# Kernel optimization log

Measured on AMD Instinct MI355X. Metric: run time of the kernel, lower is better.

Reference implementation:

```python
import jax, jax.numpy as jnp
import numpy as np

# ---- dims ----
N = 16380      # atoms
R = 819        # residues
APR = 20       # atoms per residue
K = 16         # k_neighbors
H = 64         # hidden_mult (channels)
HEADS = 8
DH = H // HEADS
L = 6          # hidden_layers
BINS = 100
MIN_D, MAX_D = 0.0, 10.0
E_DIM = 64     # embed_dim
FFN = 2 * H    # mlp_ratio = 2


def setup_inputs() -> dict:
    key = jax.random.key(0)
    ks = jax.random.split(key, 22)
    g = lambda k, shape, fan: jax.random.normal(k, shape, jnp.float32) / np.sqrt(fan)
    return {
        'coords': jax.random.uniform(ks[0], (N, 3), jnp.float32) * 70.0,
        'atom_ids': jax.random.randint(ks[1], (N,), 0, 64),
        'res_ids': jax.random.randint(ks[2], (N,), 0, 8),
        'elem_ids': jax.random.randint(ks[3], (N,), 0, 16),
        'residue_index': jnp.repeat(jnp.arange(R), APR),
        'emb_atom': jax.random.normal(ks[4], (64, 32), jnp.float32),
        'emb_res': jax.random.normal(ks[5], (8, 16), jnp.float32),
        'emb_elem': jax.random.normal(ks[6], (16, 16), jnp.float32),
        'Win': g(ks[7], (E_DIM, H), E_DIM),
        'Wq': g(ks[8], (L, H, H), H),
        'Wk': g(ks[9], (L, H, H), H),
        'Wv': g(ks[10], (L, H, H), H),
        'Wvec': g(ks[11], (L, H, H), H),
        'wdir': jax.random.normal(ks[12], (L, H), jnp.float32) * 0.1,
        'dist_bias': jax.random.normal(ks[13], (L, BINS, HEADS), jnp.float32) * 0.1,
        'Wo': g(ks[14], (L, H, H), H),
        'W1': g(ks[15], (L, H, FFN), H),
        'W2': g(ks[16], (L, FFN, H), FFN),
        'Wg': g(ks[17], (L, H, H), H),
        'Wout': g(ks[18], (H, 2), H),
        'bout': jnp.zeros((2,), jnp.float32),
    }


def _ln(x):
    m = jnp.mean(x, axis=-1, keepdims=True)
    v = jnp.mean((x - m) ** 2, axis=-1, keepdims=True)
    return (x - m) * jax.lax.rsqrt(v + 1e-5)


def reference(coords, atom_ids, res_ids, elem_ids, residue_index,
              emb_atom, emb_res, emb_elem, Win, Wq, Wk, Wv, Wvec, wdir,
              dist_bias, Wo, W1, W2, Wg, Wout, bout):
    n = coords.shape[0]
    # --- polymer embedding: concat atom/residue/element embeddings ---
    feat = jnp.concatenate(
        [emb_atom[atom_ids], emb_res[res_ids], emb_elem[elem_ids]], axis=-1)  # (N, E_DIM)
    # --- kNN graph via dense pairwise distances (avoid (N,N,3) intermediate) ---
    sq = jnp.sum(coords * coords, axis=-1)
    d2 = sq[:, None] + sq[None, :] - 2.0 * (coords @ coords.T)     # (N, N)
    idx = jnp.arange(n)
    d2 = d2.at[idx, idx].set(jnp.inf)
    _, nbr = jax.lax.top_k(-d2, K)                                  # (N, K) src per dst
    # --- edge geometry: relative vector, distance, bin ---
    dvec = coords[:, None, :] - coords[nbr]                         # (N, K, 3) dst - src
    d = jnp.sqrt(jnp.sum(dvec * dvec, axis=-1) + 1e-12)
    dirn = dvec / d[..., None]
    bins = jnp.clip(((d - MIN_D) / (MAX_D - MIN_D) * BINS).astype(jnp.int32), 0, BINS - 1)
    # --- lift to hidden repr: scalars from embedding, vectors start at zero ---
    s = feat @ Win                                                  # (N, H) l=0 features
    v = jnp.zeros((n, H, 3), s.dtype)                               # (N, H, 3) l=1 features
    for l in range(L):
        h = _ln(s)
        q = (h @ Wq[l]).reshape(n, HEADS, DH)
        kf = (h @ Wk[l]).reshape(n, HEADS, DH)
        vf = (h @ Wv[l]).reshape(n, HEADS, DH)
        kn, vn = kf[nbr], vf[nbr]                                   # (N, K, HEADS, DH)
        logits = jnp.einsum('nhd,nkhd->nkh', q, kn) / np.sqrt(DH) + dist_bias[l][bins]
        attn = jax.nn.softmax(logits, axis=1)                       # softmax over K nbrs
        msg = jnp.einsum('nkh,nkhd->nhd', attn, vn).reshape(n, H)
        # equivariant vector messages: mixed source vectors + edge direction term
        vvals = jnp.einsum('nhc,hg->ngc', v, Wvec[l])               # (N, H, 3)
        vmsg = vvals[nbr] + wdir[l][None, None, :, None] * dirn[:, :, None, :]
        attn_c = jnp.repeat(attn, DH, axis=-1)                      # (N, K, H)
        vagg = jnp.einsum('nkh,nkhc->nhc', attn_c, vmsg)
        s = s + msg @ Wo[l]
        v = v + vagg
        h2 = _ln(s)
        s = s + jax.nn.gelu(h2 @ W1[l]) @ W2[l]                     # scalar FFN
        v = v * jax.nn.sigmoid(h2 @ Wg[l])[..., None]               # gated vector update
    # --- out repr is l=0 only; residue mean-pool then linear head ---
    res_feat = jax.ops.segment_sum(s, residue_index, num_segments=R) / APR
    return res_feat @ Wout + bout                                   # (R, 2)
```

## Files before the change

### kernel.cpp

```cpp
#include <hip/hip_runtime.h>
#include <cfloat>

#define NN    16380
#define RR    819
#define APR   20
#define KNB   16
#define HID   64
#define LAYERS 6
#define BINS  100
#define N64   (NN*HID)

#define ATB   32
#define NBLK  512
#define LDA   68
#define LDU   132
#define CSIZE 4.375f

#define OFF_QA    0
#define OFF_KA    (1*N64)
#define OFF_FA    (2*N64)
#define OFF_QB    (3*N64)
#define OFF_KB    (4*N64)
#define OFF_FB    (5*N64)
#define OFF_VA    (6*N64)
#define OFF_VB    (9*N64)
#define OFF_S     (12*N64)
#define OFF_DIRNS (13*N64)
#define OFF_C4    (OFF_DIRNS + NN*48)
#define OFF_C4S   (OFF_C4 + NN*4)
#define OFF_RES   (OFF_C4S + NN*4)
#define OFF_NBRS  (OFF_RES + RR*64)
#define OFF_BINSS (OFF_NBRS + NN*16)
#define OFF_O2N   (OFF_BINSS + NN*16)
#define OFF_N2O   (OFF_O2N + NN)
#define OFF_CELL  (OFF_N2O + NN)
#define OFF_HIST  (OFF_CELL + NN)
#define OFF_CNT   (OFF_HIST + 4096)
#define OFF_BASE  (OFF_CNT + 4096)

typedef unsigned long long u64;
#define U64MAX 0xFFFFFFFFFFFFFFFFull

__device__ __forceinline__ float gelu_f(float x) {
    float x3 = x*x*x;
    float t = tanhf(0.7978845608028654f*(x + 0.044715f*x3));
    return 0.5f*x*(1.0f+t);
}
__device__ __forceinline__ float sigmoid_f(float x) {
    return 1.0f/(1.0f + expf(-x));
}
__device__ __forceinline__ int spread3(int x) {
    return (x&1) | ((x&2)<<2) | ((x&4)<<4) | ((x&8)<<6);
}
__device__ __forceinline__ unsigned sortable_u32(float f) {
    unsigned u = __float_as_uint(f);
    return u ^ ((u & 0x80000000u) ? 0xFFFFFFFFu : 0x80000000u);
}

__global__ void pad_cell_kernel(const float* __restrict__ coords, float4* __restrict__ c4,
                                int* __restrict__ cellid, int* __restrict__ hist,
                                float* __restrict__ resb, int n) {
    int i = blockIdx.x*256 + threadIdx.x;
    for (int j = i; j < RR*HID; j += 16384) resb[j] = 0.f;
    if (i >= n) return;
    float x = coords[3*i], y = coords[3*i+1], z = coords[3*i+2];
    float sq = __fadd_rn(__fadd_rn(__fmul_rn(x,x), __fmul_rn(y,y)), __fmul_rn(z,z));
    c4[i] = make_float4(x, y, z, sq);
    int cx = min(15, max(0, (int)(x * (16.0f/70.0f))));
    int cy = min(15, max(0, (int)(y * (16.0f/70.0f))));
    int cz = min(15, max(0, (int)(z * (16.0f/70.0f))));
    int m = spread3(cx) | (spread3(cy)<<1) | (spread3(cz)<<2);
    cellid[i] = m;
    atomicAdd(&hist[m], 1);
}
__global__ void scan_kernel(const int* __restrict__ hist, int* __restrict__ base) {
    __shared__ int part[256];
    int t = threadIdx.x;
    int loc[16]; int s = 0;
    #pragma unroll
    for (int e = 0; e < 16; ++e) { loc[e] = s; s += hist[t*16+e]; }
    part[t] = s;
    __syncthreads();
    if (t == 0) { int acc = 0; for (int i = 0; i < 256; ++i) { int v = part[i]; part[i] = acc; acc += v; } }
    __syncthreads();
    int off = part[t];
    #pragma unroll
    for (int e = 0; e < 16; ++e) base[t*16+e] = off + loc[e];
}
__global__ void scatter_kernel(const int* __restrict__ cellid, const int* __restrict__ base,
                               int* __restrict__ cnt, int* __restrict__ o2n,
                               int* __restrict__ n2o, const float4* __restrict__ c4,
                               float4* __restrict__ c4s, int n) {
    int i = blockIdx.x*256 + threadIdx.x;
    if (i >= n) return;
    int m = cellid[i];
    int pos = base[m] + atomicAdd(&cnt[m], 1);
    o2n[i] = pos; n2o[pos] = i;
    c4s[pos] = c4[i];
}

#define SCRATCH 1024
__global__ __launch_bounds__(256) void knn_grid_kernel(
    const float4* __restrict__ c4s, const int* __restrict__ base, const int* __restrict__ hist,
    const int* __restrict__ n2o, const int* __restrict__ o2n,
    int* __restrict__ nbr, int* __restrict__ binsO, float* __restrict__ dirn, int n)
{
    __shared__ int sIdx[4][SCRATCH];
    int tid = threadIdx.x;
    int wv = tid >> 6, lane = tid & 63;
    int i = blockIdx.x*4 + wv;
    bool valid = i < n;
    int ii = valid ? i : 0;
    float4 cd = c4s[ii];
    float sqd = cd.w;
    int cx = min(15, max(0, (int)(cd.x * (16.0f/70.0f))));
    int cy = min(15, max(0, (int)(cd.y * (16.0f/70.0f))));
    int cz = min(15, max(0, (int)(cd.z * (16.0f/70.0f))));
    u64 dlist = U64MAX;
    u64 vmax  = U64MAX;
    int* sidx = sIdx[wv];

    auto compute_pk = [&](int idx) -> u64 {
        if (idx == i) return U64MAX;
        float4 cc = c4s[idx];
        float dt = __fmul_rn(cd.x, cc.x);
        dt = __fmaf_rn(cd.y, cc.y, dt);
        dt = __fmaf_rn(cd.z, cc.z, dt);
        float key = __fsub_rn(__fadd_rn(sqd, cc.w), __fmul_rn(2.0f, dt));
        int org = n2o[idx];
        return ((u64)sortable_u32(key) << 32) | (unsigned)org;
    };

    auto process_batch = [&](int M) {
        if (M <= 0) return;
        u64 lmin = U64MAX;
        for (int p = lane; p < M; p += 64) {
            u64 pk = compute_pk(sidx[p]);
            lmin = (pk < lmin) ? pk : lmin;
        }
        u64 T = lmin;
        #pragma unroll
        for (int off = 1; off < 64; off <<= 1) {
            u64 o = __shfl_xor(T, off);
            T = (o > T) ? o : T;
        }
        for (int c0 = 0; c0 < M; c0 += 64) {
            int p = c0 + lane;
            u64 mypk = (p < M) ? compute_pk(sidx[p]) : U64MAX;
            u64 bound = (vmax < T) ? vmax : T;
            unsigned long long mask = __ballot(mypk <= bound);
            while (mask) {
                int lb = (int)__builtin_ctzll(mask);
                mask &= mask - 1;
                u64 dc = __shfl(mypk, lb);
                if (dc < vmax) {
                    u64 dp = __shfl_up(dlist, 1);
                    bool below = dc < dlist;
                    bool take  = below && (lane == 0 || dc >= dp);
                    if (lane < 16) dlist = below ? (take ? dc : dp) : dlist;
                    vmax = __shfl(dlist, 15);
                }
            }
        }
    };

    for (int R = 2; R <= 16; ++R) {
        int side = 2*R+1;
        int ncell = side*side*side;
        int M = 0;
        for (int t0 = 0; t0 < ncell; t0 += 64) {
            int t = t0 + lane;
            int cnt = 0, b = 0;
            if (t < ncell) {
                int dxc = t % side - R;
                int dyc = (t/side) % side - R;
                int dzc = t/(side*side) - R;
                int ch = max(abs(dxc), max(abs(dyc), abs(dzc)));
                bool use = (R == 2) || (ch == R);
                int x = cx+dxc, y = cy+dyc, z = cz+dzc;
                if (use && x>=0 && x<16 && y>=0 && y<16 && z>=0 && z<16) {
                    int m = spread3(x) | (spread3(y)<<1) | (spread3(z)<<2);
                    cnt = hist[m]; b = base[m];
                }
            }
            int incl = cnt;
            #pragma unroll
            for (int o = 1; o < 64; o <<= 1) { int v = __shfl_up(incl, o); if (lane >= o) incl += v; }
            int excl = incl - cnt;
            int tot = __shfl(incl, 63);
            if (M + tot > SCRATCH) { process_batch(M); M = 0; }
            for (int e = 0; e < cnt; ++e) {
                int pos = M + excl + e;
                if (pos < SCRATCH) sidx[pos] = b + e;
            }
            M = min(M + tot, SCRATCH);
        }
        process_batch(M);
        float rim = (float)R * CSIZE;
        unsigned thS = sortable_u32(rim*rim - 0.05f);
        if ((unsigned)(vmax >> 32) < thS) break;
    }
    if (valid && lane < 16) {
        int org = (int)(dlist & 0xFFFFFFFFull);
        int src = o2n[org];
        float4 cs = c4s[src];
        float dx = __fsub_rn(cd.x, cs.x);
        float dy = __fsub_rn(cd.y, cs.y);
        float dz = __fsub_rn(cd.z, cs.z);
        float ss = __fadd_rn(__fadd_rn(__fmul_rn(dx,dx), __fmul_rn(dy,dy)),
                             __fmul_rn(dz,dz));
        float dd = __fsqrt_rn(__fadd_rn(ss, 1e-12f));
        nbr[i*KNB + lane] = src;
        float bf = __fmul_rn(__fdiv_rn(dd, 10.0f), 100.0f);
        int b = (int)bf;
        b = min(max(b, 0), BINS-1);
        binsO[i*KNB + lane] = b;
        dirn[i*48 + lane*3 + 0] = __fdiv_rn(dx, dd);
        dirn[i*48 + lane*3 + 1] = __fdiv_rn(dy, dd);
        dirn[i*48 + lane*3 + 2] = __fdiv_rn(dz, dd);
    }
}

__global__ __launch_bounds__(256) void prologue_kernel(
    const int* __restrict__ aid, const int* __restrict__ rid, const int* __restrict__ eid,
    const int* __restrict__ n2o,
    const float* __restrict__ ea, const float* __restrict__ er, const float* __restrict__ ee,
    const float* __restrict__ Win, const float* __restrict__ Wq, const float* __restrict__ Wk,
    const float* __restrict__ Wv,
    float* __restrict__ sg, float* __restrict__ qout, float* __restrict__ kout,
    float* __restrict__ vfout)
{
    __shared__ __align__(16) float sS[ATB*LDA];
    __shared__ __align__(16) float sH[ATB*LDA];
    __shared__ __align__(16) float sW[4096];
    const int tid = threadIdx.x;
    const int a0 = blockIdx.x*ATB;
    const int gi = tid>>4, gj = tid&15;
    const int lrow = tid>>3, lsub = tid&7;

    auto stageW = [&](const float* W) {
        const float4* src = (const float4*)W; float4* dst = (float4*)sW;
        #pragma unroll
        for (int r = 0; r < 4; ++r) dst[tid + 256*r] = src[tid + 256*r];
    };
    auto do_gemm = [&](const float* sA, float4& c0, float4& c1) {
        const float* a0p = sA + gi*LDA;
        const float* a1p = sA + (gi+16)*LDA;
        const float* wr  = sW + gj*4;
        #pragma unroll 8
        for (int k = 0; k < 64; ++k) {
            float av0 = a0p[k], av1 = a1p[k];
            float4 w = *(const float4*)(wr + k*64);
            c0.x = fmaf(av0,w.x,c0.x); c0.y = fmaf(av0,w.y,c0.y);
            c0.z = fmaf(av0,w.z,c0.z); c0.w = fmaf(av0,w.w,c0.w);
            c1.x = fmaf(av1,w.x,c1.x); c1.y = fmaf(av1,w.y,c1.y);
            c1.z = fmaf(av1,w.z,c1.z); c1.w = fmaf(av1,w.w,c1.w);
        }
    };
    auto do_ln = [&](const float* src, float* dst) {
        const float* sp = src + lrow*LDA + lsub*8;
        float v[8]; float s1 = 0.f;
        #pragma unroll
        for (int e = 0; e < 8; ++e) { v[e] = sp[e]; s1 += v[e]; }
        s1 += __shfl_xor(s1,1); s1 += __shfl_xor(s1,2); s1 += __shfl_xor(s1,4);
        float mean = s1*(1.0f/64.0f);
        float s2 = 0.f;
        #pragma unroll
        for (int e = 0; e < 8; ++e) { float t = v[e]-mean; s2 += t*t; }
        s2 += __shfl_xor(s2,1); s2 += __shfl_xor(s2,2); s2 += __shfl_xor(s2,4);
        float sc = 1.0f/sqrtf(s2*(1.0f/64.0f)+1e-5f);
        float* dp = dst + lrow*LDA + lsub*8;
        #pragma unroll
        for (int e = 0; e < 8; ++e) dp[e] = (v[e]-mean)*sc;
    };
    auto store_g = [&](float* base, float4 c0, float4 c1) {
        int g0 = a0+gi, g1 = a0+gi+16;
        if (g0 < NN) *(float4*)(base + (size_t)g0*64 + gj*4) = c0;
        if (g1 < NN) *(float4*)(base + (size_t)g1*64 + gj*4) = c1;
    };

    {
        int ga = a0 + lrow;
        int io = (ga < NN) ? n2o[ga] : 0;
        #pragma unroll
        for (int e = 0; e < 8; ++e) {
            int c = lsub*8 + e;
            float x = 0.f;
            if (ga < NN) {
                if (c < 32)      x = ea[aid[io]*32 + c];
                else if (c < 48) x = er[rid[io]*16 + (c-32)];
                else             x = ee[eid[io]*16 + (c-48)];
            }
            sH[lrow*LDA + c] = x;
        }
    }
    __syncthreads();
    stageW(Win); __syncthreads();
    {
        float4 c0 = make_float4(0,0,0,0), c1 = c0;
        do_gemm(sH, c0, c1);
        *(float4*)(sS + gi*LDA + gj*4)      = c0;
        *(float4*)(sS + (gi+16)*LDA + gj*4) = c1;
        store_g(sg, c0, c1);
    }
    __syncthreads();
    do_ln(sS, sH);
    __syncthreads();
    stageW(Wk); __syncthreads();
    { float4 c0 = make_float4(0,0,0,0), c1 = c0; do_gemm(sH, c0, c1); store_g(kout, c0, c1); }
    __syncthreads();
    stageW(Wv); __syncthreads();
    { float4 c0 = make_float4(0,0,0,0), c1 = c0; do_gemm(sH, c0, c1); store_g(vfout, c0, c1); }
    __syncthreads();
    stageW(Wq); __syncthreads();
    { float4 c0 = make_float4(0,0,0,0), c1 = c0; do_gemm(sH, c0, c1); store_g(qout, c0, c1); }
}

__global__ __launch_bounds__(256) void layer_kernel(
    const float* __restrict__ qin, const float* __restrict__ kin, const float* __restrict__ vfin,
    float* __restrict__ qout, float* __restrict__ kout, float* __restrict__ vfout,
    const float* __restrict__ vin, float* __restrict__ vout,
    float* __restrict__ sg, const float* __restrict__ dirn,
    const int* __restrict__ nbr, const int* __restrict__ bins,
    float* __restrict__ resb, const int* __restrict__ ridx, const int* __restrict__ n2o,
    const float* __restrict__ Wvec, const float* __restrict__ wdir,
    const float* __restrict__ dist_bias,
    const float* __restrict__ Wo, const float* __restrict__ W1, const float* __restrict__ W2,
    const float* __restrict__ Wg, const float* __restrict__ Wq, const float* __restrict__ Wk,
    const float* __restrict__ Wv, int l)
{
    __shared__ __align__(16) float sS[ATB*LDA];
    __shared__ __align__(16) float sH[ATB*LDA];
    __shared__ __align__(16) float sM[ATB*LDU];
    __shared__ __align__(16) float sVA[3][ATB*LDA];
    __shared__ __align__(16) float sW[4096];
    __shared__ float sDS[ATB*24];

    const int tid = threadIdx.x;
    const int a0 = blockIdx.x*ATB;
    const int gi = tid>>4, gj = tid&15;
    const int lrow = tid>>3, lsub = tid&7;
    const int wv = tid>>6, lane = tid&63;

    const float* Wo_l = Wo + l*4096;
    const float* Wg_l = Wg + l*4096;
    const float* Wc_l = Wvec + l*4096;
    const float* W1_l = W1 + l*8192;
    const float* W2_l = W2 + l*8192;
    const float* db_l = dist_bias + l*BINS*8;
    const float* wd_l = wdir + l*64;

    auto stageW = [&](const float* W) {
        const float4* src = (const float4*)W; float4* dst = (float4*)sW;
        #pragma unroll
        for (int r = 0; r < 4; ++r) dst[tid + 256*r] = src[tid + 256*r];
    };
    auto stageW1h = [&](const float* W1l, int h) {
        const float4* src = (const float4*)W1l; float4* dst = (float4*)sW;
        #pragma unroll
        for (int r = 0; r < 4; ++r) {
            int q = tid + 256*r;
            int row = q >> 4, c4i = q & 15;
            dst[q] = src[row*32 + h*16 + c4i];
        }
    };
    auto do_gemm = [&](const float* sA, int lda, int ko, float4& c0, float4& c1) {
        const float* a0p = sA + gi*lda + ko;
        const float* a1p = sA + (gi+16)*lda + ko;
        const float* wr  = sW + gj*4;
        #pragma unroll 8
        for (int k = 0; k < 64; ++k) {
            float av0 = a0p[k], av1 = a1p[k];
            float4 w = *(const float4*)(wr + k*64);
            c0.x = fmaf(av0,w.x,c0.x); c0.y = fmaf(av0,w.y,c0.y);
            c0.z = fmaf(av0,w.z,c0.z); c0.w = fmaf(av0,w.w,c0.w);
            c1.x = fmaf(av1,w.x,c1.x); c1.y = fmaf(av1,w.y,c1.y);
            c1.z = fmaf(av1,w.z,c1.z); c1.w = fmaf(av1,w.w,c1.w);
        }
    };
    auto do_ln = [&](const float* src, float* dst) {
        const float* sp = src + lrow*LDA + lsub*8;
        float v[8]; float s1 = 0.f;
        #pragma unroll
        for (int e = 0; e < 8; ++e) { v[e] = sp[e]; s1 += v[e]; }
        s1 += __shfl_xor(s1,1); s1 += __shfl_xor(s1,2); s1 += __shfl_xor(s1,4);
        float mean = s1*(1.0f/64.0f);
        float s2 = 0.f;
        #pragma unroll
        for (int e = 0; e < 8; ++e) { float t = v[e]-mean; s2 += t*t; }
        s2 += __shfl_xor(s2,1); s2 += __shfl_xor(s2,2); s2 += __shfl_xor(s2,4);
        float sc = 1.0f/sqrtf(s2*(1.0f/64.0f)+1e-5f);
        float* dp = dst + lrow*LDA + lsub*8;
        #pragma unroll
        for (int e = 0; e < 8; ++e) dp[e] = (v[e]-mean)*sc;
    };
    auto store_g = [&](float* base, float4 c0, float4 c1) {
        int g0 = a0+gi, g1 = a0+gi+16;
        if (g0 < NN) *(float4*)(base + (size_t)g0*64 + gj*4) = c0;
        if (g1 < NN) *(float4*)(base + (size_t)g1*64 + gj*4) = c1;
    };

    {
        int ga = a0 + lrow;
        float4 z = make_float4(0,0,0,0);
        float4 x0 = z, x1 = z;
        if (ga < NN) {
            const float4* sp = (const float4*)(sg + (size_t)ga*64);
            x0 = sp[lsub*2]; x1 = sp[lsub*2+1];
        }
        float4* dp = (float4*)(sS + lrow*LDA);
        dp[lsub*2] = x0; dp[lsub*2+1] = x1;
    }

    for (int aa = 0; aa < 8; ++aa) {
        int la = wv*8 + aa;
        int ga = a0 + la;
        if (ga >= NN) break;
        float qh = qin[(size_t)ga*64 + lane];
        float lg[KNB]; int nb[KNB];
        #pragma unroll
        for (int k = 0; k < KNB; ++k) {
            int j = nbr[ga*KNB + k];
            nb[k] = j;
            float t = qh * kin[(size_t)j*64 + lane];
            t += __shfl_xor(t,1); t += __shfl_xor(t,2); t += __shfl_xor(t,4);
            lg[k] = t*0.35355339059327373f + db_l[bins[ga*KNB+k]*8 + (lane>>3)];
        }
        float m = lg[0];
        #pragma unroll
        for (int k = 1; k < KNB; ++k) m = fmaxf(m, lg[k]);
        float ssum = 0.f;
        #pragma unroll
        for (int k = 0; k < KNB; ++k) { lg[k] = expf(lg[k]-m); ssum += lg[k]; }
        float inv = 1.0f/ssum;
        float mh=0.f, b0=0.f, b1=0.f, b2=0.f, s0=0.f, s1=0.f, s2=0.f;
        if (l > 0) {
            #pragma unroll
            for (int k = 0; k < KNB; ++k) {
                float w = lg[k]*inv; int j = nb[k];
                mh += w * vfin[(size_t)j*64 + lane];
                b0 += w * vin[(size_t)j*64 + lane];
                b1 += w * vin[(size_t)N64 + (size_t)j*64 + lane];
                b2 += w * vin[2*(size_t)N64 + (size_t)j*64 + lane];
                s0 += w * dirn[ga*48 + k*3 + 0];
                s1 += w * dirn[ga*48 + k*3 + 1];
                s2 += w * dirn[ga*48 + k*3 + 2];
            }
            sVA[0][la*LDA + lane] = b0;
            sVA[1][la*LDA + lane] = b1;
            sVA[2][la*LDA + lane] = b2;
        } else {
            #pragma unroll
            for (int k = 0; k < KNB; ++k) {
                float w = lg[k]*inv; int j = nb[k];
                mh += w * vfin[(size_t)j*64 + lane];
                s0 += w * dirn[ga*48 + k*3 + 0];
                s1 += w * dirn[ga*48 + k*3 + 1];
                s2 += w * dirn[ga*48 + k*3 + 2];
            }
        }
        sM[la*LDU + lane] = mh;
        if ((lane & 7) == 0) {
            int hh = lane >> 3;
            sDS[la*24 + 0*8 + hh] = s0;
            sDS[la*24 + 1*8 + hh] = s1;
            sDS[la*24 + 2*8 + hh] = s2;
        }
    }
    __syncthreads();

    stageW(Wo_l); __syncthreads();
    {
        float4 c0 = *(float4*)(sS + gi*LDA + gj*4);
        float4 c1 = *(float4*)(sS + (gi+16)*LDA + gj*4);
        do_gemm(sM, LDU, 0, c0, c1);
        __syncthreads();
        *(float4*)(sS + gi*LDA + gj*4)      = c0;
        *(float4*)(sS + (gi+16)*LDA + gj*4) = c1;
    }
    __syncthreads();

    do_ln(sS, sH);
    __syncthreads();

    stageW(Wg_l); __syncthreads();
    {
        float4 g0 = make_float4(0,0,0,0), g1 = g0;
        do_gemm(sH, LDA, 0, g0, g1);
        g0.x=sigmoid_f(g0.x); g0.y=sigmoid_f(g0.y); g0.z=sigmoid_f(g0.z); g0.w=sigmoid_f(g0.w);
        g1.x=sigmoid_f(g1.x); g1.y=sigmoid_f(g1.y); g1.z=sigmoid_f(g1.z); g1.w=sigmoid_f(g1.w);
        __syncthreads();
        stageW(Wc_l); __syncthreads();
        float4 wd4 = *(const float4*)&wd_l[gj*4];
        int g0i = a0+gi, g1i = a0+gi+16;
        #pragma unroll
        for (int p = 0; p < 3; ++p) {
            float4 t0 = make_float4(0,0,0,0), t1 = t0;
            if (l > 0) do_gemm(sVA[p], LDA, 0, t0, t1);
            float sp0 = sDS[gi*24 + p*8 + (gj>>1)];
            float sp1 = sDS[(gi+16)*24 + p*8 + (gj>>1)];
            if (g0i < NN) {
                float4 vi = make_float4(0,0,0,0);
                if (l > 0) vi = *(const float4*)(vin + (size_t)p*N64 + (size_t)g0i*64 + gj*4);
                float4 o;
                o.x = (vi.x + t0.x + wd4.x*sp0)*g0.x;
                o.y = (vi.y + t0.y + wd4.y*sp0)*g0.y;
                o.z = (vi.z + t0.z + wd4.z*sp0)*g0.z;
                o.w = (vi.w + t0.w + wd4.w*sp0)*g0.w;
                *(float4*)(vout + (size_t)p*N64 + (size_t)g0i*64 + gj*4) = o;
            }
            if (g1i < NN) {
                float4 vi = make_float4(0,0,0,0);
                if (l > 0) vi = *(const float4*)(vin + (size_t)p*N64 + (size_t)g1i*64 + gj*4);
                float4 o;
                o.x = (vi.x + t1.x + wd4.x*sp1)*g1.x;
                o.y = (vi.y + t1.y + wd4.y*sp1)*g1.y;
                o.z = (vi.z + t1.z + wd4.z*sp1)*g1.z;
                o.w = (vi.w + t1.w + wd4.w*sp1)*g1.w;
                *(float4*)(vout + (size_t)p*N64 + (size_t)g1i*64 + gj*4) = o;
            }
        }
    }
    __syncthreads();

    stageW1h(W1_l, 0); __syncthreads();
    {
        float4 c0 = make_float4(0,0,0,0), c1 = c0;
        do_gemm(sH, LDA, 0, c0, c1);
        c0.x=gelu_f(c0.x); c0.y=gelu_f(c0.y); c0.z=gelu_f(c0.z); c0.w=gelu_f(c0.w);
        c1.x=gelu_f(c1.x); c1.y=gelu_f(c1.y); c1.z=gelu_f(c1.z); c1.w=gelu_f(c1.w);
        __syncthreads();
        *(float4*)(sM + gi*LDU + gj*4)      = c0;
        *(float4*)(sM + (gi+16)*LDU + gj*4) = c1;
    }
    __syncthreads();
    stageW1h(W1_l, 1); __syncthreads();
    {
        float4 c0 = make_float4(0,0,0,0), c1 = c0;
        do_gemm(sH, LDA, 0, c0, c1);
        c0.x=gelu_f(c0.x); c0.y=gelu_f(c0.y); c0.z=gelu_f(c0.z); c0.w=gelu_f(c0.w);
        c1.x=gelu_f(c1.x); c1.y=gelu_f(c1.y); c1.z=gelu_f(c1.z); c1.w=gelu_f(c1.w);
        __syncthreads();
        *(float4*)(sM + gi*LDU + 64 + gj*4)      = c0;
        *(float4*)(sM + (gi+16)*LDU + 64 + gj*4) = c1;
    }
    __syncthreads();
    stageW(W2_l); __syncthreads();
    {
        float4 c0 = *(float4*)(sS + gi*LDA + gj*4);
        float4 c1 = *(float4*)(sS + (gi+16)*LDA + gj*4);
        do_gemm(sM, LDU, 0, c0, c1);
        __syncthreads();
        stageW(W2_l + 4096); __syncthreads();
        do_gemm(sM, LDU, 64, c0, c1);
        __syncthreads();
        *(float4*)(sS + gi*LDA + gj*4)      = c0;
        *(float4*)(sS + (gi+16)*LDA + gj*4) = c1;
    }
    __syncthreads();

    if (l < LAYERS-1) {
        do_ln(sS, sH);
        __syncthreads();
        stageW(Wk + (l+1)*4096); __syncthreads();
        { float4 c0 = make_float4(0,0,0,0), c1 = c0; do_gemm(sH, LDA, 0, c0, c1); store_g(kout, c0, c1); }
        __syncthreads();
        stageW(Wv + (l+1)*4096); __syncthreads();
        { float4 c0 = make_float4(0,0,0,0), c1 = c0; do_gemm(sH, LDA, 0, c0, c1); store_g(vfout, c0, c1); }
        __syncthreads();
        stageW(Wq + (l+1)*4096); __syncthreads();
        { float4 c0 = make_float4(0,0,0,0), c1 = c0; do_gemm(sH, LDA, 0, c0, c1); store_g(qout, c0, c1); }
        {
            int ga = a0 + lrow;
            if (ga < NN) {
                float4* dp = (float4*)(sg + (size_t)ga*64);
                const float4* sp = (const float4*)(sS + lrow*LDA);
                dp[lsub*2] = sp[lsub*2]; dp[lsub*2+1] = sp[lsub*2+1];
            }
        }
    } else {
        int ga = a0 + lrow;
        if (ga < NN) {
            int r = ridx[n2o[ga]];
            #pragma unroll
            for (int e = 0; e < 8; ++e)
                atomicAdd(&resb[r*64 + lsub*8 + e], sS[lrow*LDA + lsub*8 + e]);
        }
    }
}

__global__ void head_kernel(const float* __restrict__ res, const float* __restrict__ Wout,
                            const float* __restrict__ bout, float* __restrict__ out, int r_total) {
    int wave = threadIdx.x >> 6, lane = threadIdx.x & 63;
    int r = blockIdx.x*4 + wave;
    if (r >= r_total) return;
    float p = res[r*HID + lane] * (1.0f/APR);
    float o0 = p * Wout[lane*2 + 0];
    float o1 = p * Wout[lane*2 + 1];
    #pragma unroll
    for (int off = 1; off < 64; off <<= 1) { o0 += __shfl_xor(o0, off); o1 += __shfl_xor(o1, off); }
    if (lane == 0) { out[r*2+0] = o0 + bout[0]; out[r*2+1] = o1 + bout[1]; }
}

extern "C" void kernel_launch(void* const* d_in, const int* in_sizes, int n_in,
                              void* d_out, int out_size, void* d_ws, size_t ws_size,
                              hipStream_t stream) {
    const float* coords    = (const float*)d_in[0];
    const int*   atom_ids  = (const int*)d_in[1];
    const int*   res_ids   = (const int*)d_in[2];
    const int*   elem_ids  = (const int*)d_in[3];
    const int*   ridx      = (const int*)d_in[4];
    const float* emb_atom  = (const float*)d_in[5];
    const float* emb_res   = (const float*)d_in[6];
    const float* emb_elem  = (const float*)d_in[7];
    const float* Win       = (const float*)d_in[8];
    const float* Wq        = (const float*)d_in[9];
    const float* Wk        = (const float*)d_in[10];
    const float* Wv        = (const float*)d_in[11];
    const float* Wvec      = (const float*)d_in[12];
    const float* wdir      = (const float*)d_in[13];
    const float* dist_bias = (const float*)d_in[14];
    const float* Wo        = (const float*)d_in[15];
    const float* W1        = (const float*)d_in[16];
    const float* W2        = (const float*)d_in[17];
    const float* Wg        = (const float*)d_in[18];
    const float* Wout      = (const float*)d_in[19];
    const float* bout      = (const float*)d_in[20];
    float* out = (float*)d_out;

    float* ws = (float*)d_ws;
    float* qA = ws + OFF_QA;  float* kA = ws + OFF_KA;  float* fA = ws + OFF_FA;
    float* qB = ws + OFF_QB;  float* kB = ws + OFF_KB;  float* fB = ws + OFF_FB;
    float* vA = ws + OFF_VA;  float* vB = ws + OFF_VB;
    float* sg = ws + OFF_S;
    float* dirn_s = ws + OFF_DIRNS;
    float4* c4  = (float4*)(ws + OFF_C4);
    float4* c4s = (float4*)(ws + OFF_C4S);
    float* resb = ws + OFF_RES;
    int* nbr_s  = (int*)(ws + OFF_NBRS);
    int* bins_s = (int*)(ws + OFF_BINSS);
    int* o2n    = (int*)(ws + OFF_O2N);
    int* n2o    = (int*)(ws + OFF_N2O);
    int* cellid = (int*)(ws + OFF_CELL);
    int* hist   = (int*)(ws + OFF_HIST);
    int* cnt    = (int*)(ws + OFF_CNT);
    int* baseb  = (int*)(ws + OFF_BASE);

    hipMemsetAsync(hist, 0, 2*4096*sizeof(int), stream);

    pad_cell_kernel<<<(NN+255)/256, 256, 0, stream>>>(coords, c4, cellid, hist, resb, NN);
    scan_kernel<<<1, 256, 0, stream>>>(hist, baseb);
    scatter_kernel<<<(NN+255)/256, 256, 0, stream>>>(cellid, baseb, cnt, o2n, n2o, c4, c4s, NN);
    knn_grid_kernel<<<(NN+3)/4, 256, 0, stream>>>(c4s, baseb, hist, n2o, o2n, nbr_s, bins_s, dirn_s, NN);

    prologue_kernel<<<NBLK, 256, 0, stream>>>(atom_ids, res_ids, elem_ids, n2o,
                                              emb_atom, emb_res, emb_elem,
                                              Win, Wq, Wk, Wv, sg, qA, kA, fA);
    for (int l = 0; l < LAYERS; ++l) {
        int p = l & 1;
        const float* qin = p ? qB : qA;  float* qout = p ? qA : qB;
        const float* kin = p ? kB : kA;  float* kout = p ? kA : kB;
        const float* fin = p ? fB : fA;  float* fout = p ? fA : fB;
        const float* vin = p ? vB : vA;  float* vout = p ? vA : vB;
        layer_kernel<<<NBLK, 256, 0, stream>>>(qin, kin, fin, qout, kout, fout,
                                               vin, vout, sg, dirn_s, nbr_s, bins_s,
                                               resb, ridx, n2o,
                                               Wvec, wdir, dist_bias,
                                               Wo, W1, W2, Wg, Wq, Wk, Wv, l);
    }
    head_kernel<<<(RR+3)/4, 256, 0, stream>>>(resb, Wout, bout, out, RR);
}
```

Baseline: 648.7 us.

## Alias LDS buffers and compute vector-mix GEMM early to raise occupancy

Merges sH, sW and the three sVA buffers into one aliased shared array, cutting LDS per block so more blocks can be resident, and adds a min-blocks hint of 3 to launch_bounds. To make the aliasing safe, the Wvec GEMM on the aggregated vector features now runs right after aggregation, reading Wvec straight from global memory. Its 24 accumulators are held in registers until the gated update. This keeps more registers live across the Wo/LN/Wg phases, which the occupancy hint may force into spills, and the weight reads now go through cache instead of LDS.

```diff
diff --git a/kernel.cpp b/kernel.cpp
--- a/kernel.cpp
+++ b/kernel.cpp
@@ -316,7 +316,7 @@
     { float4 c0 = make_float4(0,0,0,0), c1 = c0; do_gemm(sH, c0, c1); store_g(qout, c0, c1); }
 }
 
-__global__ __launch_bounds__(256) void layer_kernel(
+__global__ __launch_bounds__(256, 3) void layer_kernel(
     const float* __restrict__ qin, const float* __restrict__ kin, const float* __restrict__ vfin,
     float* __restrict__ qout, float* __restrict__ kout, float* __restrict__ vfout,
     const float* __restrict__ vin, float* __restrict__ vout,
@@ -330,11 +330,11 @@
     const float* __restrict__ Wv, int l)
 {
     __shared__ __align__(16) float sS[ATB*LDA];
-    __shared__ __align__(16) float sH[ATB*LDA];
     __shared__ __align__(16) float sM[ATB*LDU];
-    __shared__ __align__(16) float sVA[3][ATB*LDA];
-    __shared__ __align__(16) float sW[4096];
     __shared__ float sDS[ATB*24];
+    __shared__ __align__(16) float sX[6272];
+    float* sH = sX;
+    float* sW = sX + 2176;
 
     const int tid = threadIdx.x;
     const int a0 = blockIdx.x*ATB;
@@ -446,9 +446,9 @@
                 s1 += w * dirn[ga*48 + k*3 + 1];
                 s2 += w * dirn[ga*48 + k*3 + 2];
             }
-            sVA[0][la*LDA + lane] = b0;
-            sVA[1][la*LDA + lane] = b1;
-            sVA[2][la*LDA + lane] = b2;
+            sX[0*2048 + la*64 + lane] = b0;
+            sX[1*2048 + la*64 + lane] = b1;
+            sX[2*2048 + la*64 + lane] = b2;
         } else {
             #pragma unroll
             for (int k = 0; k < KNB; ++k) {
@@ -469,6 +469,28 @@
     }
     __syncthreads();
 
+    float4 t0[3], t1[3];
+    #pragma unroll
+    for (int p = 0; p < 3; ++p) { t0[p] = make_float4(0,0,0,0); t1[p] = make_float4(0,0,0,0); }
+    if (l > 0) {
+        #pragma unroll
+        for (int p = 0; p < 3; ++p) {
+            const float* a0p = sX + p*2048 + gi*64;
+            const float* a1p = sX + p*2048 + (gi+16)*64;
+            const float* wr  = Wc_l + gj*4;
+            #pragma unroll 8
+            for (int k = 0; k < 64; ++k) {
+                float av0 = a0p[k], av1 = a1p[k];
+                float4 w = *(const float4*)(wr + k*64);
+                t0[p].x = fmaf(av0,w.x,t0[p].x); t0[p].y = fmaf(av0,w.y,t0[p].y);
+                t0[p].z = fmaf(av0,w.z,t0[p].z); t0[p].w = fmaf(av0,w.w,t0[p].w);
+                t1[p].x = fmaf(av1,w.x,t1[p].x); t1[p].y = fmaf(av1,w.y,t1[p].y);
+                t1[p].z = fmaf(av1,w.z,t1[p].z); t1[p].w = fmaf(av1,w.w,t1[p].w);
+            }
+        }
+    }
+    __syncthreads();
+
     stageW(Wo_l); __syncthreads();
     {
         float4 c0 = *(float4*)(sS + gi*LDA + gj*4);
@@ -489,34 +511,30 @@
         do_gemm(sH, LDA, 0, g0, g1);
         g0.x=sigmoid_f(g0.x); g0.y=sigmoid_f(g0.y); g0.z=sigmoid_f(g0.z); g0.w=sigmoid_f(g0.w);
         g1.x=sigmoid_f(g1.x); g1.y=sigmoid_f(g1.y); g1.z=sigmoid_f(g1.z); g1.w=sigmoid_f(g1.w);
-        __syncthreads();
-        stageW(Wc_l); __syncthreads();
         float4 wd4 = *(const float4*)&wd_l[gj*4];
         int g0i = a0+gi, g1i = a0+gi+16;
         #pragma unroll
         for (int p = 0; p < 3; ++p) {
-            float4 t0 = make_float4(0,0,0,0), t1 = t0;
-            if (l > 0) do_gemm(sVA[p], LDA, 0, t0, t1);
             float sp0 = sDS[gi*24 + p*8 + (gj>>1)];
             float sp1 = sDS[(gi+16)*24 + p*8 + (gj>>1)];
             if (g0i < NN) {
                 float4 vi = make_float4(0,0,0,0);
                 if (l > 0) vi = *(const float4*)(vin + (size_t)p*N64 + (size_t)g0i*64 + gj*4);
                 float4 o;
-                o.x = (vi.x + t0.x + wd4.x*sp0)*g0.x;
-                o.y = (vi.y + t0.y + wd4.y*sp0)*g0.y;
-                o.z = (vi.z + t0.z + wd4.z*sp0)*g0.z;
-                o.w = (vi.w + t0.w + wd4.w*sp0)*g0.w;
+                o.x = (vi.x + t0[p].x + wd4.x*sp0)*g0.x;
+                o.y = (vi.y + t0[p].y + wd4.y*sp0)*g0.y;
+                o.z = (vi.z + t0[p].z + wd4.z*sp0)*g0.z;
+                o.w = (vi.w + t0[p].w + wd4.w*sp0)*g0.w;
                 *(float4*)(vout + (size_t)p*N64 + (size_t)g0i*64 + gj*4) = o;
             }
             if (g1i < NN) {
                 float4 vi = make_float4(0,0,0,0);
                 if (l > 0) vi = *(const float4*)(vin + (size_t)p*N64 + (size_t)g1i*64 + gj*4);
                 float4 o;
-                o.x = (vi.x + t1.x + wd4.x*sp1)*g1.x;
-                o.y = (vi.y + t1.y + wd4.y*sp1)*g1.y;
-                o.z = (vi.z + t1.z + wd4.z*sp1)*g1.z;
-                o.w = (vi.w + t1.w + wd4.w*sp1)*g1.w;
+                o.x = (vi.x + t1[p].x + wd4.x*sp1)*g1.x;
+                o.y = (vi.y + t1[p].y + wd4.y*sp1)*g1.y;
+                o.z = (vi.z + t1[p].z + wd4.z*sp1)*g1.z;
+                o.w = (vi.w + t1[p].w + wd4.w*sp1)*g1.w;
                 *(float4*)(vout + (size_t)p*N64 + (size_t)g1i*64 + gj*4) = o;
             }
         }
```

New measurement: 994.2 us. +53.3%, slower.

## Halve atoms per block in layer kernel, keep residual in registers, swizzle blocks

Applied to the files above, without the earlier changes.

The layer kernel now processes 16 atoms per block across 1024 blocks instead of 32 across 512. Each thread owns one float4 of the residual stream in registers, so the shared sS buffer and its extra syncs and copies go away. LayerNorm is done in registers with shuffles, blocks are remapped with a strided swizzle, and launch bounds request 3 blocks per CU. This raises parallelism and occupancy and cuts LDS use. In exchange, every block restages the full weight matrices for half the atoms, doubling weight-staging traffic per atom.

```diff
diff --git a/kernel.cpp b/kernel.cpp
--- a/kernel.cpp
+++ b/kernel.cpp
@@ -12,6 +12,8 @@
 
 #define ATB   32
 #define NBLK  512
+#define ATB2  16
+#define NBLK2 1024
 #define LDA   68
 #define LDU   132
 #define CSIZE 4.375f
@@ -316,7 +318,7 @@
     { float4 c0 = make_float4(0,0,0,0), c1 = c0; do_gemm(sH, c0, c1); store_g(qout, c0, c1); }
 }
 
-__global__ __launch_bounds__(256) void layer_kernel(
+__global__ __launch_bounds__(256, 3) void layer_kernel(
     const float* __restrict__ qin, const float* __restrict__ kin, const float* __restrict__ vfin,
     float* __restrict__ qout, float* __restrict__ kout, float* __restrict__ vfout,
     const float* __restrict__ vin, float* __restrict__ vout,
@@ -329,18 +331,18 @@
     const float* __restrict__ Wg, const float* __restrict__ Wq, const float* __restrict__ Wk,
     const float* __restrict__ Wv, int l)
 {
-    __shared__ __align__(16) float sS[ATB*LDA];
-    __shared__ __align__(16) float sH[ATB*LDA];
-    __shared__ __align__(16) float sM[ATB*LDU];
-    __shared__ __align__(16) float sVA[3][ATB*LDA];
+    __shared__ __align__(16) float sH[ATB2*LDA];
+    __shared__ __align__(16) float sM[ATB2*LDU];
+    __shared__ __align__(16) float sVA[3][ATB2*LDA];
     __shared__ __align__(16) float sW[4096];
-    __shared__ float sDS[ATB*24];
+    __shared__ float sDS[ATB2*24];
 
     const int tid = threadIdx.x;
-    const int a0 = blockIdx.x*ATB;
+    const int bswz = (blockIdx.x & 7) * (NBLK2/8) + (blockIdx.x >> 3);
+    const int a0 = bswz*ATB2;
     const int gi = tid>>4, gj = tid&15;
-    const int lrow = tid>>3, lsub = tid&7;
     const int wv = tid>>6, lane = tid&63;
+    const int ga = a0 + gi;
 
     const float* Wo_l = Wo + l*4096;
     const float* Wg_l = Wg + l*4096;
@@ -364,67 +366,44 @@
             dst[q] = src[row*32 + h*16 + c4i];
         }
     };
-    auto do_gemm = [&](const float* sA, int lda, int ko, float4& c0, float4& c1) {
-        const float* a0p = sA + gi*lda + ko;
-        const float* a1p = sA + (gi+16)*lda + ko;
-        const float* wr  = sW + gj*4;
+    auto do_gemm = [&](const float* sA, int lda, int ko, float4& c) {
+        const float* ap = sA + gi*lda + ko;
+        const float* wr = sW + gj*4;
         #pragma unroll 8
         for (int k = 0; k < 64; ++k) {
-            float av0 = a0p[k], av1 = a1p[k];
+            float av = ap[k];
             float4 w = *(const float4*)(wr + k*64);
-            c0.x = fmaf(av0,w.x,c0.x); c0.y = fmaf(av0,w.y,c0.y);
-            c0.z = fmaf(av0,w.z,c0.z); c0.w = fmaf(av0,w.w,c0.w);
-            c1.x = fmaf(av1,w.x,c1.x); c1.y = fmaf(av1,w.y,c1.y);
-            c1.z = fmaf(av1,w.z,c1.z); c1.w = fmaf(av1,w.w,c1.w);
-        }
-    };
-    auto do_ln = [&](const float* src, float* dst) {
-        const float* sp = src + lrow*LDA + lsub*8;
-        float v[8]; float s1 = 0.f;
-        #pragma unroll
-        for (int e = 0; e < 8; ++e) { v[e] = sp[e]; s1 += v[e]; }
-        s1 += __shfl_xor(s1,1); s1 += __shfl_xor(s1,2); s1 += __shfl_xor(s1,4);
+            c.x = fmaf(av,w.x,c.x); c.y = fmaf(av,w.y,c.y);
+            c.z = fmaf(av,w.z,c.z); c.w = fmaf(av,w.w,c.w);
+        }
+    };
+    auto ln_reg = [&](float4 v) {
+        float s1 = v.x+v.y+v.z+v.w;
+        s1 += __shfl_xor(s1,1); s1 += __shfl_xor(s1,2); s1 += __shfl_xor(s1,4); s1 += __shfl_xor(s1,8);
         float mean = s1*(1.0f/64.0f);
-        float s2 = 0.f;
-        #pragma unroll
-        for (int e = 0; e < 8; ++e) { float t = v[e]-mean; s2 += t*t; }
-        s2 += __shfl_xor(s2,1); s2 += __shfl_xor(s2,2); s2 += __shfl_xor(s2,4);
+        float t0=v.x-mean, t1=v.y-mean, t2=v.z-mean, t3=v.w-mean;
+        float s2 = t0*t0+t1*t1+t2*t2+t3*t3;
+        s2 += __shfl_xor(s2,1); s2 += __shfl_xor(s2,2); s2 += __shfl_xor(s2,4); s2 += __shfl_xor(s2,8);
         float sc = 1.0f/sqrtf(s2*(1.0f/64.0f)+1e-5f);
-        float* dp = dst + lrow*LDA + lsub*8;
-        #pragma unroll
-        for (int e = 0; e < 8; ++e) dp[e] = (v[e]-mean)*sc;
-    };
-    auto store_g = [&](float* base, float4 c0, float4 c1) {
-        int g0 = a0+gi, g1 = a0+gi+16;
-        if (g0 < NN) *(float4*)(base + (size_t)g0*64 + gj*4) = c0;
-        if (g1 < NN) *(float4*)(base + (size_t)g1*64 + gj*4) = c1;
-    };
-
-    {
-        int ga = a0 + lrow;
-        float4 z = make_float4(0,0,0,0);
-        float4 x0 = z, x1 = z;
-        if (ga < NN) {
-            const float4* sp = (const float4*)(sg + (size_t)ga*64);
-            x0 = sp[lsub*2]; x1 = sp[lsub*2+1];
-        }
-        float4* dp = (float4*)(sS + lrow*LDA);
-        dp[lsub*2] = x0; dp[lsub*2+1] = x1;
-    }
-
-    for (int aa = 0; aa < 8; ++aa) {
-        int la = wv*8 + aa;
-        int ga = a0 + la;
-        if (ga >= NN) break;
-        float qh = qin[(size_t)ga*64 + lane];
+        *(float4*)(sH + gi*LDA + gj*4) = make_float4(t0*sc, t1*sc, t2*sc, t3*sc);
+    };
+
+    float4 sreg = make_float4(0,0,0,0);
+    if (ga < NN) sreg = *(const float4*)(sg + (size_t)ga*64 + gj*4);
+
+    for (int aa = 0; aa < 4; ++aa) {
+        int la = wv*4 + aa;
+        int gaa = a0 + la;
+        if (gaa >= NN) break;
+        float qh = qin[(size_t)gaa*64 + lane];
         float lg[KNB]; int nb[KNB];
         #pragma unroll
         for (int k = 0; k < KNB; ++k) {
-            int j = nbr[ga*KNB + k];
+            int j = nbr[gaa*KNB + k];
             nb[k] = j;
             float t = qh * kin[(size_t)j*64 + lane];
             t += __shfl_xor(t,1); t += __shfl_xor(t,2); t += __shfl_xor(t,4);
-            lg[k] = t*0.35355339059327373f + db_l[bins[ga*KNB+k]*8 + (lane>>3)];
+            lg[k] = t*0.35355339059327373f + db_l[bins[gaa*KNB+k]*8 + (lane>>3)];
         }
         float m = lg[0];
         #pragma unroll
@@ -442,9 +421,9 @@
                 b0 += w * vin[(size_t)j*64 + lane];
                 b1 += w * vin[(size_t)N64 + (size_t)j*64 + lane];
                 b2 += w * vin[2*(size_t)N64 + (size_t)j*64 + lane];
-                s0 += w * dirn[ga*48 + k*3 + 0];
-                s1 += w * dirn[ga*48 + k*3 + 1];
-                s2 += w * dirn[ga*48 + k*3 + 2];
+                s0 += w * dirn[gaa*48 + k*3 + 0];
+                s1 += w * dirn[gaa*48 + k*3 + 1];
+                s2 += w * dirn[gaa*48 + k*3 + 2];
             }
             sVA[0][la*LDA + lane] = b0;
             sVA[1][la*LDA + lane] = b1;
@@ -454,9 +433,9 @@
             for (int k = 0; k < KNB; ++k) {
                 float w = lg[k]*inv; int j = nb[k];
                 mh += w * vfin[(size_t)j*64 + lane];
-                s0 += w * dirn[ga*48 + k*3 + 0];
-                s1 += w * dirn[ga*48 + k*3 + 1];
-                s2 += w * dirn[ga*48 + k*3 + 2];
+                s0 += w * dirn[gaa*48 + k*3 + 0];
+                s1 += w * dirn[gaa*48 + k*3 + 1];
+                s2 += w * dirn[gaa*48 + k*3 + 2];
             }
         }
         sM[la*LDU + lane] = mh;
@@ -470,54 +449,32 @@
     __syncthreads();
 
     stageW(Wo_l); __syncthreads();
-    {
-        float4 c0 = *(float4*)(sS + gi*LDA + gj*4);
-        float4 c1 = *(float4*)(sS + (gi+16)*LDA + gj*4);
-        do_gemm(sM, LDU, 0, c0, c1);
-        __syncthreads();
-        *(float4*)(sS + gi*LDA + gj*4)      = c0;
-        *(float4*)(sS + (gi+16)*LDA + gj*4) = c1;
-    }
-    __syncthreads();
-
-    do_ln(sS, sH);
+    do_gemm(sM, LDU, 0, sreg);
+    ln_reg(sreg);
     __syncthreads();
 
     stageW(Wg_l); __syncthreads();
     {
-        float4 g0 = make_float4(0,0,0,0), g1 = g0;
-        do_gemm(sH, LDA, 0, g0, g1);
-        g0.x=sigmoid_f(g0.x); g0.y=sigmoid_f(g0.y); g0.z=sigmoid_f(g0.z); g0.w=sigmoid_f(g0.w);
-        g1.x=sigmoid_f(g1.x); g1.y=sigmoid_f(g1.y); g1.z=sigmoid_f(g1.z); g1.w=sigmoid_f(g1.w);
+        float4 g = make_float4(0,0,0,0);
+        do_gemm(sH, LDA, 0, g);
+        g.x=sigmoid_f(g.x); g.y=sigmoid_f(g.y); g.z=sigmoid_f(g.z); g.w=sigmoid_f(g.w);
         __syncthreads();
         stageW(Wc_l); __syncthreads();
         float4 wd4 = *(const float4*)&wd_l[gj*4];
-        int g0i = a0+gi, g1i = a0+gi+16;
         #pragma unroll
         for (int p = 0; p < 3; ++p) {
-            float4 t0 = make_float4(0,0,0,0), t1 = t0;
-            if (l > 0) do_gemm(sVA[p], LDA, 0, t0, t1);
-            float sp0 = sDS[gi*24 + p*8 + (gj>>1)];
-            float sp1 = sDS[(gi+16)*24 + p*8 + (gj>>1)];
-            if (g0i < NN) {
+            float4 t = make_float4(0,0,0,0);
+            if (l > 0) do_gemm(sVA[p], LDA, 0, t);
+            float sp = sDS[gi*24 + p*8 + (gj>>1)];
+            if (ga < NN) {
                 float4 vi = make_float4(0,0,0,0);
-                if (l > 0) vi = *(const float4*)(vin + (size_t)p*N64 + (size_t)g0i*64 + gj*4);
+                if (l > 0) vi = *(const float4*)(vin + (size_t)p*N64 + (size_t)ga*64 + gj*4);
                 float4 o;
-                o.x = (vi.x + t0.x + wd4.x*sp0)*g0.x;
-                o.y = (vi.y + t0.y + wd4.y*sp0)*g0.y;
-                o.z = (vi.z + t0.z + wd4.z*sp0)*g0.z;
-                o.w = (vi.w + t0.w + wd4.w*sp0)*g0.w;
-                *(float4*)(vout + (size_t)p*N64 + (size_t)g0i*64 + gj*4) = o;
-            }
-            if (g1i < NN) {
-                float4 vi = make_float4(0,0,0,0);
-                if (l > 0) vi = *(const float4*)(vin + (size_t)p*N64 + (size_t)g1i*64 + gj*4);
-                float4 o;
-                o.x = (vi.x + t1.x + wd4.x*sp1)*g1.x;
-                o.y = (vi.y + t1.y + wd4.y*sp1)*g1.y;
-                o.z = (vi.z + t1.z + wd4.z*sp1)*g1.z;
-                o.w = (vi.w + t1.w + wd4.w*sp1)*g1.w;
-                *(float4*)(vout + (size_t)p*N64 + (size_t)g1i*64 + gj*4) = o;
+                o.x = (vi.x + t.x + wd4.x*sp)*g.x;
+                o.y = (vi.y + t.y + wd4.y*sp)*g.y;
+                o.z = (vi.z + t.z + wd4.z*sp)*g.z;
+                o.w = (vi.w + t.w + wd4.w*sp)*g.w;
+                *(float4*)(vout + (size_t)p*N64 + (size_t)ga*64 + gj*4) = o;
             }
         }
     }
@@ -525,66 +482,49 @@
 
     stageW1h(W1_l, 0); __syncthreads();
     {
-        float4 c0 = make_float4(0,0,0,0), c1 = c0;
-        do_gemm(sH, LDA, 0, c0, c1);
-        c0.x=gelu_f(c0.x); c0.y=gelu_f(c0.y); c0.z=gelu_f(c0.z); c0.w=gelu_f(c0.w);
-        c1.x=gelu_f(c1.x); c1.y=gelu_f(c1.y); c1.z=gelu_f(c1.z); c1.w=gelu_f(c1.w);
-        __syncthreads();
-        *(float4*)(sM + gi*LDU + gj*4)      = c0;
-        *(float4*)(sM + (gi+16)*LDU + gj*4) = c1;
+        float4 c = make_float4(0,0,0,0);
+        do_gemm(sH, LDA, 0, c);
+        c.x=gelu_f(c.x); c.y=gelu_f(c.y); c.z=gelu_f(c.z); c.w=gelu_f(c.w);
+        *(float4*)(sM + gi*LDU + gj*4) = c;
     }
     __syncthreads();
     stageW1h(W1_l, 1); __syncthreads();
     {
-        float4 c0 = make_float4(0,0,0,0), c1 = c0;
-        do_gemm(sH, LDA, 0, c0, c1);
-        c0.x=gelu_f(c0.x); c0.y=gelu_f(c0.y); c0.z=gelu_f(c0.z); c0.w=gelu_f(c0.w);
-        c1.x=gelu_f(c1.x); c1.y=gelu_f(c1.y); c1.z=gelu_f(c1.z); c1.w=gelu_f(c1.w);
-        __syncthreads();
-        *(float4*)(sM + gi*LDU + 64 + gj*4)      = c0;
-        *(float4*)(sM + (gi+16)*LDU + 64 + gj*4) = c1;
+        float4 c = make_float4(0,0,0,0);
+        do_gemm(sH, LDA, 0, c);
+        c.x=gelu_f(c.x); c.y=gelu_f(c.y); c.z=gelu_f(c.z); c.w=gelu_f(c.w);
+        *(float4*)(sM + gi*LDU + 64 + gj*4) = c;
     }
     __syncthreads();
     stageW(W2_l); __syncthreads();
-    {
-        float4 c0 = *(float4*)(sS + gi*LDA + gj*4);
-        float4 c1 = *(float4*)(sS + (gi+16)*LDA + gj*4);
-        do_gemm(sM, LDU, 0, c0, c1);
-        __syncthreads();
-        stageW(W2_l + 4096); __syncthreads();
-        do_gemm(sM, LDU, 64, c0, c1);
-        __syncthreads();
-        *(float4*)(sS + gi*LDA + gj*4)      = c0;
-        *(float4*)(sS + (gi+16)*LDA + gj*4) = c1;
-    }
+    do_gemm(sM, LDU, 0, sreg);
+    __syncthreads();
+    stageW(W2_l + 4096); __syncthreads();
+    do_gemm(sM, LDU, 64, sreg);
     __syncthreads();
 
     if (l < LAYERS-1) {
-        do_ln(sS, sH);
+        ln_reg(sreg);
+        if (ga < NN) *(float4*)(sg + (size_t)ga*64 + gj*4) = sreg;
         __syncthreads();
         stageW(Wk + (l+1)*4096); __syncthreads();
-        { float4 c0 = make_float4(0,0,0,0), c1 = c0; do_gemm(sH, LDA, 0, c0, c1); store_g(kout, c0, c1); }
+        { float4 c = make_float4(0,0,0,0); do_gemm(sH, LDA, 0, c);
+          if (ga < NN) *(float4*)(kout + (size_t)ga*64 + gj*4) = c; }
         __syncthreads();
         stageW(Wv + (l+1)*4096); __syncthreads();
-        { float4 c0 = make_float4(0,0,0,0), c1 = c0; do_gemm(sH, LDA, 0, c0, c1); store_g(vfout, c0, c1); }
+        { float4 c = make_float4(0,0,0,0); do_gemm(sH, LDA, 0, c);
+          if (ga < NN) *(float4*)(vfout + (size_t)ga*64 + gj*4) = c; }
         __syncthreads();
         stageW(Wq + (l+1)*4096); __syncthreads();
-        { float4 c0 = make_float4(0,0,0,0), c1 = c0; do_gemm(sH, LDA, 0, c0, c1); store_g(qout, c0, c1); }
-        {
-            int ga = a0 + lrow;
-            if (ga < NN) {
-                float4* dp = (float4*)(sg + (size_t)ga*64);
-                const float4* sp = (const float4*)(sS + lrow*LDA);
-                dp[lsub*2] = sp[lsub*2]; dp[lsub*2+1] = sp[lsub*2+1];
-            }
-        }
+        { float4 c = make_float4(0,0,0,0); do_gemm(sH, LDA, 0, c);
+          if (ga < NN) *(float4*)(qout + (size_t)ga*64 + gj*4) = c; }
     } else {
-        int ga = a0 + lrow;
         if (ga < NN) {
             int r = ridx[n2o[ga]];
-            #pragma unroll
-            for (int e = 0; e < 8; ++e)
-                atomicAdd(&resb[r*64 + lsub*8 + e], sS[lrow*LDA + lsub*8 + e]);
+            atomicAdd(&resb[r*64 + gj*4 + 0], sreg.x);
+            atomicAdd(&resb[r*64 + gj*4 + 1], sreg.y);
+            atomicAdd(&resb[r*64 + gj*4 + 2], sreg.z);
+            atomicAdd(&resb[r*64 + gj*4 + 3], sreg.w);
         }
     }
 }
@@ -662,11 +602,11 @@
         const float* kin = p ? kB : kA;  float* kout = p ? kA : kB;
         const float* fin = p ? fB : fA;  float* fout = p ? fA : fB;
         const float* vin = p ? vB : vA;  float* vout = p ? vA : vB;
-        layer_kernel<<<NBLK, 256, 0, stream>>>(qin, kin, fin, qout, kout, fout,
-                                               vin, vout, sg, dirn_s, nbr_s, bins_s,
-                                               resb, ridx, n2o,
-                                               Wvec, wdir, dist_bias,
-                                               Wo, W1, W2, Wg, Wq, Wk, Wv, l);
+        layer_kernel<<<NBLK2, 256, 0, stream>>>(qin, kin, fin, qout, kout, fout,
+                                                vin, vout, sg, dirn_s, nbr_s, bins_s,
+                                                resb, ridx, n2o,
+                                                Wvec, wdir, dist_bias,
+                                                Wo, W1, W2, Wg, Wq, Wk, Wv, l);
     }
     head_kernel<<<(RR+3)/4, 256, 0, stream>>>(resb, Wout, bout, out, RR);
 }
```

Measured after the change: 888.2 us. 36.9% more time.
